# Kernel optimization log

Measured on AMD Instinct MI355X. Metric: run time of the kernel, lower is better.

Reference implementation:

```python
import jax, jax.numpy as jnp
import numpy as np

N = 50000   # nodes
E = 800000  # edges
G = 64      # graphs in batch
D = 128     # num_input
H = 128     # num_hidden
O = 10      # num_output


def _linear_params(key, fan_in, fan_out):
    k1, k2 = jax.random.split(key)
    s = 1.0 / np.sqrt(fan_in)
    W = jax.random.uniform(k1, (fan_out, fan_in), jnp.float32, -s, s)
    b = jax.random.uniform(k2, (fan_out,), jnp.float32, -s, s)
    return W, b


def setup_inputs() -> dict:
    key = jax.random.key(0)
    ks = jax.random.split(key, 12)
    x = jax.random.normal(ks[0], (N, D), jnp.float32)
    edge_index = jax.random.randint(ks[1], (2, E), 0, N, dtype=jnp.int32).astype(jnp.int64)
    batch = jnp.sort(jax.random.randint(ks[2], (N,), 0, G, dtype=jnp.int32)).astype(jnp.int64)

    W_rel1, b_rel1 = _linear_params(ks[3], D, H)
    W_root1, _ = _linear_params(ks[4], D, H)
    W_rel2, b_rel2 = _linear_params(ks[5], H, H)
    W_root2, _ = _linear_params(ks[6], H, H)
    W_rel3, b_rel3 = _linear_params(ks[7], H, H)
    W_root3, _ = _linear_params(ks[8], H, H)
    W1, b1 = _linear_params(ks[9], 2 * H, 128)
    W2, b2 = _linear_params(ks[10], 128, 64)
    W3, b3 = _linear_params(ks[11], 64, O)

    return dict(x=x, edge_index=edge_index, batch=batch,
                W_rel1=W_rel1, b_rel1=b_rel1, W_root1=W_root1,
                W_rel2=W_rel2, b_rel2=b_rel2, W_root2=W_root2,
                W_rel3=W_rel3, b_rel3=b_rel3, W_root3=W_root3,
                W1=W1, b1=b1, W2=W2, b2=b2, W3=W3, b3=b3)


def _graph_conv(x, src, dst, W_rel, b_rel, W_root):
    # PyG GraphConv (aggr='add'): out_i = W_rel @ sum_{j->i} x_j + b_rel + W_root @ x_i
    agg = jax.ops.segment_sum(x[src], dst, num_segments=N)  # [N, d]
    return agg @ W_rel.T + b_rel + x @ W_root.T


def _pool(x, batch):
    # concat(global_max_pool, global_mean_pool) -> [G, 2d]
    mx = jax.ops.segment_max(x, batch, num_segments=G)
    mx = jnp.where(jnp.isfinite(mx), mx, 0.0)  # guard empty segments
    sm = jax.ops.segment_sum(x, batch, num_segments=G)
    cnt = jax.ops.segment_sum(jnp.ones((x.shape[0], 1), x.dtype), batch, num_segments=G)
    mean = sm / jnp.maximum(cnt, 1.0)
    return jnp.concatenate([mx, mean], axis=1)


def reference(x, edge_index, batch,
              W_rel1, b_rel1, W_root1,
              W_rel2, b_rel2, W_root2,
              W_rel3, b_rel3, W_root3,
              W1, b1, W2, b2, W3, b3):
    src, dst = edge_index[0], edge_index[1]
    h = jax.nn.relu(_graph_conv(x, src, dst, W_rel1, b_rel1, W_root1))
    x1 = _pool(h, batch)
    h = jax.nn.relu(_graph_conv(h, src, dst, W_rel2, b_rel2, W_root2))
    x2 = _pool(h, batch)
    h = jax.nn.relu(_graph_conv(h, src, dst, W_rel3, b_rel3, W_root3))
    x3 = _pool(h, batch)
    node_embs = h
    graph_emb = x1 + x2 + x3           # [G, 2H]
    z = jax.nn.relu(graph_emb @ W1.T + b1)
    z = jax.nn.relu(z @ W2.T + b2)     # dropout p=0 -> no-op
    logits = z @ W3.T + b3             # [G, O]
    return logits, node_embs, graph_emb
```

## Files before the change

### kernel.cpp

```cpp
#include <hip/hip_runtime.h>
#include <hip/hip_bf16.h>

#define NN 50000
#define EE 800000
#define GG 64
#define NBUCK 196
#define ABLOCKS 125
#define CHUNK 6400
#define BCAP 8192

typedef __attribute__((ext_vector_type(8))) short bf16x8;
typedef __attribute__((ext_vector_type(4))) float f32x4;

__device__ __forceinline__ float bflo(unsigned u) { return __uint_as_float(u << 16); }
__device__ __forceinline__ float bfhi(unsigned u) { return __uint_as_float(u & 0xffff0000u); }
__device__ __forceinline__ float b2f(unsigned short s) { return __uint_as_float(((unsigned)s) << 16); }
__device__ __forceinline__ unsigned short f2bf(float f) {
    __hip_bfloat16 h = __float2bfloat16(f);
    union { __hip_bfloat16 h; unsigned short u; } cv; cv.h = h; return cv.u;
}

__global__ void detect_kernel(const unsigned* __restrict__ xw,
                              const unsigned* __restrict__ eiw,
                              int* __restrict__ flags) {
    __shared__ int s_cnt, s_nz;
    if (threadIdx.x == 0) { s_cnt = 0; s_nz = 0; }
    __syncthreads();
    int cnt = 0;
    for (int i = threadIdx.x; i < 4096; i += 256) {
        unsigned w = xw[(size_t)i * 711];
        unsigned elo = (w >> 7) & 0xFF;
        if (elo >= 100 && elo <= 140) cnt++;
    }
    int nz = 0;
    for (int i = threadIdx.x; i < 1024; i += 256) {
        unsigned w = eiw[(size_t)i * 1560 + 1];
        if (w != 0) nz++;
    }
    atomicAdd(&s_cnt, cnt);
    atomicAdd(&s_nz, nz);
    __syncthreads();
    if (threadIdx.x == 0) {
        flags[0] = (s_cnt < 3600) ? 1 : 0;
        flags[1] = (s_nz  < 8)    ? 1 : 0;
    }
}

struct WPtrs { const void* p[15]; };

__global__ __launch_bounds__(256) void prep_kernel(const void* __restrict__ xsrc,
                                                   const unsigned* __restrict__ eiw,
                                                   WPtrs wp,
                                                   unsigned short* __restrict__ arena,
                                                   int* __restrict__ counts,
                                                   uint4* __restrict__ zero_region,
                                                   const int* __restrict__ flags) {
    const int b = blockIdx.x;
    const int tid = threadIdx.x;
    const int isF32 = flags[0];

    if (b < 3125) {
        const int total4 = NN * 128 / 4;
        for (int i = b * 256 + tid; i < total4; i += 800000) {
            uint2 o;
            if (isF32) {
                float4 f = ((const float4*)xsrc)[i];
                o.x = (unsigned)f2bf(f.x) | ((unsigned)f2bf(f.y) << 16);
                o.y = (unsigned)f2bf(f.z) | ((unsigned)f2bf(f.w) << 16);
            } else {
                o = ((const uint2*)xsrc)[i];
            }
            ((uint2*)arena)[i] = o;
        }
    } else if (b < 3674) {
        const int cnt[15] = {16384,128,16384, 16384,128,16384, 16384,128,16384,
                             32768,128,8192,64,640,10};
        const int dst[15] = {19200000,19232768,19216384, 19232896,19265664,19249280,
                             19265792,19298560,19282176,
                             19298688,19331456,19331584,19339776,19339840,19340480};
        const int total = 140490;
        int i = (b - 3125) * 256 + tid;
        if (i < total) {
            int seg = 0, base = 0;
            while (i - base >= cnt[seg]) { base += cnt[seg]; ++seg; }
            int off = i - base;
            const void* s = wp.p[seg];
            arena[dst[seg] + off] =
                isF32 ? f2bf(((const float*)s)[off]) : ((const unsigned short*)s)[off];
        }
    } else if (b < 3799) {
        __shared__ int hist[256];
        hist[tid] = 0;
        __syncthreads();
        const int i64 = flags[1];
        const int e0 = (b - 3674) * CHUNK;
        for (int it = 0; it < CHUNK / 256; ++it) {
            int e = e0 + it * 256 + tid;
            int d = (int)(i64 ? eiw[(size_t)2 * (EE + e)] : eiw[EE + e]);
            atomicAdd(&hist[d >> 8], 1);
        }
        __syncthreads();
        counts[(b - 3674) * 256 + tid] = hist[tid];
    } else {
        zero_region[(b - 3799) * 256 + tid] = (uint4){0, 0, 0, 0};
    }
}

__global__ __launch_bounds__(256) void bucket_offsets(const int* __restrict__ counts,
                                                      int* __restrict__ offsets,
                                                      int* __restrict__ bucket_base) {
    __shared__ int s[256];
    const int t = threadIdx.x;
    int col = 0;
    for (int b = 0; b < ABLOCKS; ++b) col += counts[b * 256 + t];
    s[t] = col;
    __syncthreads();
    for (int d = 1; d < 256; d <<= 1) {
        int x = (t >= d) ? s[t - d] : 0;
        __syncthreads();
        s[t] += x;
        __syncthreads();
    }
    int base = s[t] - col;
    bucket_base[t] = base;
    if (t == 255) bucket_base[256] = s[255];
    int run = base;
    for (int b = 0; b < ABLOCKS; ++b) {
        offsets[b * 256 + t] = run;
        run += counts[b * 256 + t];
    }
}

__global__ __launch_bounds__(256) void bucket_scatter(const unsigned* __restrict__ eiw,
                                                      const int* __restrict__ offsets,
                                                      unsigned* __restrict__ packed,
                                                      const int* __restrict__ flags) {
    __shared__ int cur[256];
    cur[threadIdx.x] = offsets[blockIdx.x * 256 + threadIdx.x];
    __syncthreads();
    int i64 = flags[1];
    int e0 = blockIdx.x * CHUNK;
    for (int it = 0; it < CHUNK / 256; ++it) {
        int e = e0 + it * 256 + threadIdx.x;
        int s = (int)(i64 ? eiw[(size_t)2 * e]        : eiw[e]);
        int d = (int)(i64 ? eiw[(size_t)2 * (EE + e)] : eiw[EE + e]);
        int pos = atomicAdd(&cur[d >> 8], 1);
        packed[pos] = ((unsigned)s << 8) | (unsigned)(d & 255);
    }
}

__global__ __launch_bounds__(256) void bucket_sort(const unsigned* __restrict__ packed,
                                                   const int* __restrict__ bucket_base,
                                                   int* __restrict__ csr_src,
                                                   int* __restrict__ row_ptr) {
    __shared__ unsigned sbuf[BCAP];
    __shared__ int hist[256];
    __shared__ int cur[256];
    const int t = threadIdx.x;
    const int b = blockIdx.x;
    const int lo = bucket_base[b];
    int n = bucket_base[b + 1] - lo;
    if (n > BCAP) n = BCAP;

    hist[t] = 0;
    __syncthreads();
    for (int i = t; i < n; i += 256) {
        unsigned p = packed[lo + i];
        sbuf[i] = p;
        atomicAdd(&hist[p & 255], 1);
    }
    __syncthreads();
    int v = hist[t];
    __shared__ int s[256];
    s[t] = v;
    __syncthreads();
    for (int d = 1; d < 256; d <<= 1) {
        int x = (t >= d) ? s[t - d] : 0;
        __syncthreads();
        s[t] += x;
        __syncthreads();
    }
    int start = s[t] - v;
    int node = b * 256 + t;
    if (node < NN) row_ptr[node] = lo + start;
    if (b == 0 && t == 0) row_ptr[NN] = EE;
    cur[t] = start;
    __syncthreads();
    for (int i = t; i < n; i += 256) {
        unsigned p = sbuf[i];
        int pos = atomicAdd(&cur[p & 255], 1);
        csr_src[lo + pos] = (int)(p >> 8);
    }
}

__global__ __launch_bounds__(256, 8) void conv_fused(const unsigned short* __restrict__ hin,
                                                     const int* __restrict__ row_ptr,
                                                     const int* __restrict__ csr_src,
                                                     const unsigned short* __restrict__ Wrel,
                                                     const unsigned short* __restrict__ Wroot,
                                                     const unsigned short* __restrict__ brel,
                                                     const unsigned* __restrict__ bw,
                                                     unsigned* __restrict__ pmx,
                                                     float* __restrict__ psum,
                                                     unsigned short* __restrict__ outb,
                                                     void* __restrict__ outG,
                                                     const int* __restrict__ flags) {
    __shared__ __align__(16) unsigned short tile[16][136];
    __shared__ int sbatch[16];

    const int tid  = threadIdx.x;
    const int wv   = tid >> 6;
    const int lane = tid & 63;
    const int half = lane >> 5;
    const int l32  = lane & 31;
    const int m0   = blockIdx.x * 16;
    const uint2* h8 = (const uint2*)hin;

    for (int i = 0; i < 4; ++i) {
        const int lr = wv * 4 + i;
        const int r  = m0 + lr;
        float ax = 0.f, ay = 0.f, az = 0.f, aw = 0.f;
        int jb = row_ptr[r], je = row_ptr[r + 1];
        int j = jb + half;
        for (; j + 14 < je; j += 16) {
            uint2 u[8];
            #pragma unroll
            for (int q = 0; q < 8; ++q)
                u[q] = h8[(size_t)csr_src[j + 2 * q] * 32 + l32];
            #pragma unroll
            for (int q = 0; q < 8; ++q) {
                ax += bflo(u[q].x); ay += bfhi(u[q].x);
                az += bflo(u[q].y); aw += bfhi(u[q].y);
            }
        }
        for (; j + 6 < je; j += 8) {
            uint2 u[4];
            #pragma unroll
            for (int q = 0; q < 4; ++q)
                u[q] = h8[(size_t)csr_src[j + 2 * q] * 32 + l32];
            #pragma unroll
            for (int q = 0; q < 4; ++q) {
                ax += bflo(u[q].x); ay += bfhi(u[q].x);
                az += bflo(u[q].y); aw += bfhi(u[q].y);
            }
        }
        for (; j < je; j += 2) {
            uint2 u = h8[(size_t)csr_src[j] * 32 + l32];
            ax += bflo(u.x); ay += bfhi(u.x);
            az += bflo(u.y); aw += bfhi(u.y);
        }
        ax += __shfl_xor(ax, 32);
        ay += __shfl_xor(ay, 32);
        az += __shfl_xor(az, 32);
        aw += __shfl_xor(aw, 32);
        if (half == 0) {
            uint2 o;
            o.x = (unsigned)f2bf(ax) | ((unsigned)f2bf(ay) << 16);
            o.y = (unsigned)f2bf(az) | ((unsigned)f2bf(aw) << 16);
            *(uint2*)&tile[lr][l32 * 4] = o;
        }
    }
    __syncthreads();

    const int mrow = lane & 15;
    const int quad = lane >> 4;
    const int r    = m0 + mrow;

    f32x4 acc[2];
    acc[0] = (f32x4){0.f, 0.f, 0.f, 0.f};
    acc[1] = (f32x4){0.f, 0.f, 0.f, 0.f};

    #pragma unroll
    for (int kk = 0; kk < 8; ++kk) {
        const unsigned short* Bs = (kk < 4) ? Wrel : Wroot;
        const int kc = (kk & 3) * 32 + quad * 8;
        bf16x8 a;
        if (kk < 4) a = *(const bf16x8*)&tile[mrow][kc];
        else        a = *(const bf16x8*)(hin + (size_t)r * 128 + kc);
        #pragma unroll
        for (int n = 0; n < 2; ++n) {
            const int col0 = (wv * 2 + n) * 16;
            bf16x8 b = *(const bf16x8*)(Bs + (size_t)(col0 + mrow) * 128 + kc);
            acc[n] = __builtin_amdgcn_mfma_f32_16x16x32_bf16(a, b, acc[n], 0, 0, 0);
        }
    }

    __syncthreads();

    const int isF32 = flags[0];
    #pragma unroll
    for (int n = 0; n < 2; ++n) {
        const int col = (wv * 2 + n) * 16 + mrow;
        const float bias = b2f(brel[col]);
        #pragma unroll
        for (int i = 0; i < 4; ++i) {
            const int lrow = quad * 4 + i;
            const int row  = m0 + lrow;
            float v = fmaxf(acc[n][i] + bias, 0.f);
            unsigned short bv = f2bf(v);
            outb[(size_t)row * 128 + col] = bv;
            tile[lrow][col] = bv;
            if (outG) {
                size_t o = (size_t)640 + (size_t)row * 128 + col;
                if (isF32) ((float*)outG)[o] = __uint_as_float((unsigned)bv << 16);
                else       ((unsigned short*)outG)[o] = bv;
            }
        }
    }

    const int i64 = flags[1];
    if (tid < 16) {
        int rr = m0 + tid;
        sbatch[tid] = (int)(i64 ? bw[(size_t)2 * rr] : bw[rr]);
    }
    __syncthreads();
    if (tid < 128) {
        const int col = tid;
        const int slice = blockIdx.x & 7;
        int curg = sbatch[0];
        float mx = 0.f, sm = 0.f;
        for (int rr = 0; rr < 16; ++rr) {
            int g = sbatch[rr];
            if (g != curg) {
                atomicMax(&pmx[(slice * GG + curg) * 128 + col], __float_as_uint(mx));
                unsafeAtomicAdd(&psum[(slice * GG + curg) * 128 + col], sm);
                curg = g; mx = 0.f; sm = 0.f;
            }
            float v = b2f(tile[rr][col]);
            mx = fmaxf(mx, v);
            sm += v;
        }
        atomicMax(&pmx[(slice * GG + curg) * 128 + col], __float_as_uint(mx));
        unsafeAtomicAdd(&psum[(slice * GG + curg) * 128 + col], sm);
    }
}

__global__ __launch_bounds__(256) void mlp_kernel(const unsigned* __restrict__ pmxL,
                                                  const float* __restrict__ psum,
                                                  const unsigned* __restrict__ bw,
                                                  const unsigned short* __restrict__ W1,
                                                  const unsigned short* __restrict__ b1,
                                                  const unsigned short* __restrict__ W2,
                                                  const unsigned short* __restrict__ b2,
                                                  const unsigned short* __restrict__ W3,
                                                  const unsigned short* __restrict__ b3,
                                                  void* __restrict__ out,
                                                  const int* __restrict__ flags) {
    int g = blockIdx.x;
    int t = threadIdx.x;
    int isF32 = flags[0];
    int i64 = flags[1];
    __shared__ float sge[256];
    __shared__ float sz1[128];
    __shared__ float sz2[64];

    int lo = 0, hi = NN;
    while (lo < hi) {
        int mid = (lo + hi) >> 1;
        int bv = (int)(i64 ? bw[(size_t)2 * mid] : bw[mid]);
        if (bv < g) lo = mid + 1; else hi = mid;
    }
    int start = lo;
    hi = NN;
    while (lo < hi) {
        int mid = (lo + hi) >> 1;
        int bv = (int)(i64 ? bw[(size_t)2 * mid] : bw[mid]);
        if (bv < g + 1) lo = mid + 1; else hi = mid;
    }
    int cnt = lo - start;

    float v;
    if (t < 128) {
        v = 0.f;
        #pragma unroll
        for (int L = 0; L < 3; ++L) {
            float m = 0.f;
            #pragma unroll
            for (int s = 0; s < 8; ++s)
                m = fmaxf(m, __uint_as_float(pmxL[((L * 8 + s) * GG + g) * 128 + t]));
            v += m;
        }
    } else {
        float sm = 0.f;
        #pragma unroll
        for (int s = 0; s < 8; ++s) sm += psum[(s * GG + g) * 128 + (t - 128)];
        v = sm / fmaxf((float)cnt, 1.f);
    }
    sge[t] = v;
    size_t geo = (size_t)640 + (size_t)NN * 128 + (size_t)g * 256 + t;
    if (isF32) ((float*)out)[geo] = v;
    else       ((unsigned short*)out)[geo] = f2bf(v);
    __syncthreads();

    if (t < 128) {
        float acc = b2f(b1[t]);
        for (int k = 0; k < 256; ++k) acc = fmaf(sge[k], b2f(W1[t * 256 + k]), acc);
        sz1[t] = fmaxf(acc, 0.f);
    }
    __syncthreads();
    if (t < 64) {
        float acc = b2f(b2[t]);
        for (int k = 0; k < 128; ++k) acc = fmaf(sz1[k], b2f(W2[t * 128 + k]), acc);
        sz2[t] = fmaxf(acc, 0.f);
    }
    __syncthreads();
    if (t < 10) {
        float acc = b2f(b3[t]);
        for (int k = 0; k < 64; ++k) acc = fmaf(sz2[k], b2f(W3[t * 64 + k]), acc);
        size_t o = (size_t)g * 10 + t;
        if (isF32) ((float*)out)[o] = acc;
        else       ((unsigned short*)out)[o] = f2bf(acc);
    }
}

#define XBF_OFF   0
#define HA_OFF    6400000
#define HB_OFF    12800000
#define WR1_OFF   19200000
#define WO1_OFF   19216384
#define BR1_OFF   19232768
#define WR2_OFF   19232896
#define WO2_OFF   19249280
#define BR2_OFF   19265664
#define WR3_OFF   19265792
#define WO3_OFF   19282176
#define BR3_OFF   19298560
#define W1_OFF    19298688
#define B1_OFF    19331456
#define W2_OFF    19331584
#define B2_OFF    19339776
#define W3_OFF    19339840
#define B3_OFF    19340480
#define ARENA_END 19340490

extern "C" void kernel_launch(void* const* d_in, const int* in_sizes, int n_in,
                              void* d_out, int out_size, void* d_ws, size_t ws_size,
                              hipStream_t stream) {
    unsigned short* arena = (unsigned short*)d_ws;
    size_t intBase = ((size_t)ARENA_END * 2 + 255) & ~(size_t)255;
    char* ib = (char*)d_ws + intBase;
    int*      row_ptr = (int*)ib;
    int*      csr_src = (int*)(ib + 200064);
    unsigned* packed  = (unsigned*)(ib + 3400064);
    int*      counts  = (int*)(ib + 6600064);
    int*      offsets = (int*)(ib + 6728064);
    int*      bbase   = (int*)(ib + 6856064);
    unsigned* pmxL    = (unsigned*)(ib + 6857344);
    float*    psum    = (float*)(ib + 7643776);
    int*      flags   = (int*)(ib + 7905920);

    const unsigned* eiw = (const unsigned*)d_in[1];
    const unsigned* bw  = (const unsigned*)d_in[2];
    dim3 blk(256);

    detect_kernel<<<1, 256, 0, stream>>>((const unsigned*)d_in[0], eiw, flags);

    WPtrs wp;
    for (int i = 0; i < 15; ++i) wp.p[i] = d_in[3 + i];
    prep_kernel<<<4055, blk, 0, stream>>>(d_in[0], eiw, wp, arena, counts,
                                          (uint4*)pmxL, flags);

    bucket_offsets<<<1, blk, 0, stream>>>(counts, offsets, bbase);
    bucket_scatter<<<ABLOCKS, blk, 0, stream>>>(eiw, offsets, packed, flags);
    bucket_sort<<<NBUCK, blk, 0, stream>>>(packed, bbase, csr_src, row_ptr);

    const int convGrid = NN / 16;

    conv_fused<<<convGrid, blk, 0, stream>>>(arena + XBF_OFF, row_ptr, csr_src,
                                             arena + WR1_OFF, arena + WO1_OFF, arena + BR1_OFF,
                                             bw, pmxL, psum, arena + HA_OFF, nullptr, flags);
    conv_fused<<<convGrid, blk, 0, stream>>>(arena + HA_OFF, row_ptr, csr_src,
                                             arena + WR2_OFF, arena + WO2_OFF, arena + BR2_OFF,
                                             bw, pmxL + 65536, psum, arena + HB_OFF, nullptr, flags);
    conv_fused<<<convGrid, blk, 0, stream>>>(arena + HB_OFF, row_ptr, csr_src,
                                             arena + WR3_OFF, arena + WO3_OFF, arena + BR3_OFF,
                                             bw, pmxL + 131072, psum, arena + XBF_OFF, d_out, flags);

    mlp_kernel<<<GG, blk, 0, stream>>>(pmxL, psum, bw,
                                       arena + W1_OFF, arena + B1_OFF,
                                       arena + W2_OFF, arena + B2_OFF,
                                       arena + W3_OFF, arena + B3_OFF, d_out, flags);
}
```

Baseline: 390.0 us.

## Split neighbor gather into column-group kernel separate from MFMA conv

Each fused conv kernel is split into a standalone gather kernel and an MFMA kernel. The gather kernel is grid-partitioned into four 32-feature column groups (blockIdx / 3125), so that each pass touches only a quarter of every source row, which may improve L2 hit rates for the random neighbor accesses. The gathered aggregate goes to a global buffer that the MFMA kernel then reads. This adds an extra launch and a global write and read of the N×128 aggregate per layer, and each gather pass re-reads csr_src and row_ptr four times.

After: 454.6 us. 1.17x slower.

```diff
diff --git a/kernel.cpp b/kernel.cpp
--- a/kernel.cpp
+++ b/kernel.cpp
@@ -193,77 +193,57 @@
     }
 }
 
-__global__ __launch_bounds__(256, 8) void conv_fused(const unsigned short* __restrict__ hin,
-                                                     const int* __restrict__ row_ptr,
-                                                     const int* __restrict__ csr_src,
-                                                     const unsigned short* __restrict__ Wrel,
-                                                     const unsigned short* __restrict__ Wroot,
-                                                     const unsigned short* __restrict__ brel,
-                                                     const unsigned* __restrict__ bw,
-                                                     unsigned* __restrict__ pmx,
-                                                     float* __restrict__ psum,
-                                                     unsigned short* __restrict__ outb,
-                                                     void* __restrict__ outG,
-                                                     const int* __restrict__ flags) {
+__global__ __launch_bounds__(256) void gather_cg(const unsigned* __restrict__ hin2,
+                                                 const int* __restrict__ row_ptr,
+                                                 const int* __restrict__ csr_src,
+                                                 unsigned* __restrict__ agg2) {
+    const int bid = blockIdx.x;
+    const int cg  = bid / 3125;
+    const int rb  = (bid - cg * 3125) * 16;
+    const int qw  = threadIdx.x >> 4;
+    const int l16 = threadIdx.x & 15;
+    const int r   = rb + qw;
+
+    const unsigned* base = hin2 + cg * 16 + l16;
+    int jb = row_ptr[r], je = row_ptr[r + 1];
+    float ax = 0.f, ay = 0.f;
+    int j = jb;
+    for (; j + 8 <= je; j += 8) {
+        unsigned u[8];
+        #pragma unroll
+        for (int q = 0; q < 8; ++q)
+            u[q] = base[(size_t)csr_src[j + q] * 64];
+        #pragma unroll
+        for (int q = 0; q < 8; ++q) { ax += bflo(u[q]); ay += bfhi(u[q]); }
+    }
+    for (; j < je; ++j) {
+        unsigned u = base[(size_t)csr_src[j] * 64];
+        ax += bflo(u); ay += bfhi(u);
+    }
+    agg2[(size_t)r * 64 + cg * 16 + l16] =
+        (unsigned)f2bf(ax) | ((unsigned)f2bf(ay) << 16);
+}
+
+__global__ __launch_bounds__(256, 8) void conv_mfma(const unsigned short* __restrict__ hin,
+                                                    const unsigned short* __restrict__ agg,
+                                                    const unsigned short* __restrict__ Wrel,
+                                                    const unsigned short* __restrict__ Wroot,
+                                                    const unsigned short* __restrict__ brel,
+                                                    const unsigned* __restrict__ bw,
+                                                    unsigned* __restrict__ pmx,
+                                                    float* __restrict__ psum,
+                                                    unsigned short* __restrict__ outb,
+                                                    void* __restrict__ outG,
+                                                    const int* __restrict__ flags) {
     __shared__ __align__(16) unsigned short tile[16][136];
     __shared__ int sbatch[16];
 
     const int tid  = threadIdx.x;
     const int wv   = tid >> 6;
     const int lane = tid & 63;
-    const int half = lane >> 5;
-    const int l32  = lane & 31;
-    const int m0   = blockIdx.x * 16;
-    const uint2* h8 = (const uint2*)hin;
-
-    for (int i = 0; i < 4; ++i) {
-        const int lr = wv * 4 + i;
-        const int r  = m0 + lr;
-        float ax = 0.f, ay = 0.f, az = 0.f, aw = 0.f;
-        int jb = row_ptr[r], je = row_ptr[r + 1];
-        int j = jb + half;
-        for (; j + 14 < je; j += 16) {
-            uint2 u[8];
-            #pragma unroll
-            for (int q = 0; q < 8; ++q)
-                u[q] = h8[(size_t)csr_src[j + 2 * q] * 32 + l32];
-            #pragma unroll
-            for (int q = 0; q < 8; ++q) {
-                ax += bflo(u[q].x); ay += bfhi(u[q].x);
-                az += bflo(u[q].y); aw += bfhi(u[q].y);
-            }
-        }
-        for (; j + 6 < je; j += 8) {
-            uint2 u[4];
-            #pragma unroll
-            for (int q = 0; q < 4; ++q)
-                u[q] = h8[(size_t)csr_src[j + 2 * q] * 32 + l32];
-            #pragma unroll
-            for (int q = 0; q < 4; ++q) {
-                ax += bflo(u[q].x); ay += bfhi(u[q].x);
-                az += bflo(u[q].y); aw += bfhi(u[q].y);
-            }
-        }
-        for (; j < je; j += 2) {
-            uint2 u = h8[(size_t)csr_src[j] * 32 + l32];
-            ax += bflo(u.x); ay += bfhi(u.x);
-            az += bflo(u.y); aw += bfhi(u.y);
-        }
-        ax += __shfl_xor(ax, 32);
-        ay += __shfl_xor(ay, 32);
-        az += __shfl_xor(az, 32);
-        aw += __shfl_xor(aw, 32);
-        if (half == 0) {
-            uint2 o;
-            o.x = (unsigned)f2bf(ax) | ((unsigned)f2bf(ay) << 16);
-            o.y = (unsigned)f2bf(az) | ((unsigned)f2bf(aw) << 16);
-            *(uint2*)&tile[lr][l32 * 4] = o;
-        }
-    }
-    __syncthreads();
-
     const int mrow = lane & 15;
     const int quad = lane >> 4;
+    const int m0   = blockIdx.x * 16;
     const int r    = m0 + mrow;
 
     f32x4 acc[2];
@@ -272,11 +252,10 @@
 
     #pragma unroll
     for (int kk = 0; kk < 8; ++kk) {
+        const unsigned short* As = (kk < 4) ? agg  : hin;
         const unsigned short* Bs = (kk < 4) ? Wrel : Wroot;
         const int kc = (kk & 3) * 32 + quad * 8;
-        bf16x8 a;
-        if (kk < 4) a = *(const bf16x8*)&tile[mrow][kc];
-        else        a = *(const bf16x8*)(hin + (size_t)r * 128 + kc);
+        bf16x8 a = *(const bf16x8*)(As + (size_t)r * 128 + kc);
         #pragma unroll
         for (int n = 0; n < 2; ++n) {
             const int col0 = (wv * 2 + n) * 16;
@@ -284,8 +263,6 @@
             acc[n] = __builtin_amdgcn_mfma_f32_16x16x32_bf16(a, b, acc[n], 0, 0, 0);
         }
     }
-
-    __syncthreads();
 
     const int isF32 = flags[0];
     #pragma unroll
@@ -464,17 +441,24 @@
     bucket_scatter<<<ABLOCKS, blk, 0, stream>>>(eiw, offsets, packed, flags);
     bucket_sort<<<NBUCK, blk, 0, stream>>>(packed, bbase, csr_src, row_ptr);
 
-    const int convGrid = NN / 16;
-
-    conv_fused<<<convGrid, blk, 0, stream>>>(arena + XBF_OFF, row_ptr, csr_src,
-                                             arena + WR1_OFF, arena + WO1_OFF, arena + BR1_OFF,
-                                             bw, pmxL, psum, arena + HA_OFF, nullptr, flags);
-    conv_fused<<<convGrid, blk, 0, stream>>>(arena + HA_OFF, row_ptr, csr_src,
-                                             arena + WR2_OFF, arena + WO2_OFF, arena + BR2_OFF,
-                                             bw, pmxL + 65536, psum, arena + HB_OFF, nullptr, flags);
-    conv_fused<<<convGrid, blk, 0, stream>>>(arena + HB_OFF, row_ptr, csr_src,
-                                             arena + WR3_OFF, arena + WO3_OFF, arena + BR3_OFF,
-                                             bw, pmxL + 131072, psum, arena + XBF_OFF, d_out, flags);
+    const int gatherGrid = 4 * 3125;
+    const int convGrid   = NN / 16;
+
+    gather_cg<<<gatherGrid, blk, 0, stream>>>((const unsigned*)(arena + XBF_OFF), row_ptr,
+                                              csr_src, (unsigned*)(arena + HB_OFF));
+    conv_mfma<<<convGrid, blk, 0, stream>>>(arena + XBF_OFF, arena + HB_OFF,
+                                            arena + WR1_OFF, arena + WO1_OFF, arena + BR1_OFF,
+                                            bw, pmxL, psum, arena + HA_OFF, nullptr, flags);
+    gather_cg<<<gatherGrid, blk, 0, stream>>>((const unsigned*)(arena + HA_OFF), row_ptr,
+                                              csr_src, (unsigned*)(arena + XBF_OFF));
+    conv_mfma<<<convGrid, blk, 0, stream>>>(arena + HA_OFF, arena + XBF_OFF,
+                                            arena + WR2_OFF, arena + WO2_OFF, arena + BR2_OFF,
+                                            bw, pmxL + 65536, psum, arena + HB_OFF, nullptr, flags);
+    gather_cg<<<gatherGrid, blk, 0, stream>>>((const unsigned*)(arena + HB_OFF), row_ptr,
+                                              csr_src, (unsigned*)(arena + HA_OFF));
+    conv_mfma<<<convGrid, blk, 0, stream>>>(arena + HB_OFF, arena + HA_OFF,
+                                            arena + WR3_OFF, arena + WO3_OFF, arena + BR3_OFF,
+                                            bw, pmxL + 131072, psum, arena + XBF_OFF, d_out, flags);
 
     mlp_kernel<<<GG, blk, 0, stream>>>(pmxL, psum, bw,
                                        arena + W1_OFF, arena + B1_OFF,
```
